# Kernel tuning notes

Hardware: AMD Instinct MI355X
Metric: run time of the kernel (lower is better)

Reference implementation:

```python
import jax, jax.numpy as jnp
import numpy as np

N = 100000   # nodes
E = 3200000  # edges (avg degree 32)
IN, H, OUT = 128, 256, 40
EPS = 1e-5


def _glorot(key, fan_in, fan_out):
    s = jnp.sqrt(2.0 / (fan_in + fan_out))
    return jax.random.normal(key, (fan_in, fan_out), jnp.float32) * s


def setup_inputs() -> dict:
    key = jax.random.key(0)
    ks = jax.random.split(key, 6)
    edge_index = jax.random.randint(ks[0], (2, E), 0, N, dtype=jnp.int64)
    z = jax.random.normal(ks[1], (N, IN), jnp.float32) * 0.1
    return {
        "edge_index": edge_index,
        "z": z,
        "W1": _glorot(ks[2], IN, H), "b1": jnp.zeros((H,), jnp.float32),
        "g1": jnp.ones((H,), jnp.float32), "beta1": jnp.zeros((H,), jnp.float32),
        "W2": _glorot(ks[3], H, H), "b2": jnp.zeros((H,), jnp.float32),
        "g2": jnp.ones((H,), jnp.float32), "beta2": jnp.zeros((H,), jnp.float32),
        "W3": _glorot(ks[4], H, OUT), "b3": jnp.zeros((OUT,), jnp.float32),
    }


def _gcn_norm(edge_index):
    # add self-loops, compute symmetric normalization D^-1/2 (A+I) D^-1/2
    loops = jnp.arange(N, dtype=edge_index.dtype)
    src = jnp.concatenate([edge_index[0], loops])
    dst = jnp.concatenate([edge_index[1], loops])
    deg = jax.ops.segment_sum(jnp.ones_like(dst, jnp.float32), dst, num_segments=N)
    dinv = jnp.where(deg > 0, jax.lax.rsqrt(deg), 0.0)
    norm = dinv[src] * dinv[dst]  # [E+N]
    return src, dst, norm


def _conv(x, W, b, src, dst, norm):
    h = x @ W                              # [N, F_out]
    msg = h[src] * norm[:, None]           # gather + scale, [E+N, F_out]
    return jax.ops.segment_sum(msg, dst, num_segments=N) + b


def _bn(x, g, beta):
    m = x.mean(axis=0)
    v = x.var(axis=0)  # biased variance (training-mode BatchNorm)
    return (x - m) * jax.lax.rsqrt(v + EPS) * g + beta


def reference(edge_index, z, W1, b1, g1, beta1, W2, b2, g2, beta2, W3, b3):
    src, dst, norm = _gcn_norm(edge_index)
    x = jax.nn.relu(_bn(_conv(z, W1, b1, src, dst, norm), g1, beta1))
    x = jax.nn.relu(_bn(_conv(x, W2, b2, src, dst, norm), g2, beta2))
    return _conv(x, W3, b3, src, dst, norm)  # [N, OUT]
```

## Files before the change

### kernel.cpp

```cpp
#include <hip/hip_runtime.h>


#define NN   100000
#define NE   3200000
#define FIN  128
#define FH   256
#define FOUT 40
#define EPSV 1e-5f

#define BSH   7
#define NBKT  ((NN + 127) >> BSH)
#define CAPB  8192
#define CHNK  4096

typedef __attribute__((ext_vector_type(8))) short bf8;
typedef __attribute__((ext_vector_type(4))) float f32x4;

__device__ __forceinline__ unsigned short f2bf(float x) {
    unsigned int u = __float_as_uint(x);
    unsigned int r = u + 0x7fffu + ((u >> 16) & 1u);
    return (unsigned short)(r >> 16);
}
__device__ __forceinline__ float bf2f(unsigned short h) {
    return __uint_as_float(((unsigned int)h) << 16);
}
__device__ __forceinline__ void f2bf2(float x, unsigned short& hi, unsigned short& lo) {
    unsigned short h = f2bf(x);
    hi = h;
    lo = f2bf(x - bf2f(h));
}
__device__ __forceinline__ float ub(unsigned int u, int k) {
    return (float)((u >> (8 * k)) & 0xffu);
}
__device__ __forceinline__ float sbyte(unsigned int u, int k) {
    return (float)(int)(signed char)((u >> (8 * k)) & 0xffu);
}

__global__ __launch_bounds__(256) void k_bin(const int* __restrict__ ei,
                                             int* __restrict__ gcur,
                                             unsigned int* __restrict__ staging) {
    __shared__ int hcnt[NBKT];
    __shared__ int hbase[NBKT];
    __shared__ int sflag;
    const int tid = threadIdx.x;
    const int e0 = blockIdx.x * CHNK;
    for (int b = tid; b < NBKT; b += 256) hcnt[b] = 0;
    if (tid == 0) {
        int zz = 0;
        for (int i = 0; i < 64; i++) zz |= ei[2 * i + 1];
        sflag = (zz == 0) ? 1 : 0;
    }
    __syncthreads();
    const int f = sflag;
    for (int r = 0; r < CHNK / 256; r++) {
        int e = e0 + r * 256 + tid;
        if (e < NE) {
            int d = f ? ei[2 * (NE + e)] : ei[NE + e];
            atomicAdd(&hcnt[d >> BSH], 1);
        }
    }
    __syncthreads();
    for (int b = tid; b < NBKT; b += 256) {
        int c = hcnt[b];
        hbase[b] = c ? atomicAdd(&gcur[b], c) : 0;
    }
    __syncthreads();
    for (int b = tid; b < NBKT; b += 256) hcnt[b] = 0;
    __syncthreads();
    for (int r = 0; r < CHNK / 256; r++) {
        int e = e0 + r * 256 + tid;
        if (e < NE) {
            int s = f ? ei[2 * e] : ei[e];
            int d = f ? ei[2 * (NE + e)] : ei[NE + e];
            int b = d >> BSH;
            int loc = atomicAdd(&hcnt[b], 1);
            int pos = hbase[b] + loc;
            if (pos < CAPB)
                staging[(size_t)b * CAPB + pos] =
                    (unsigned int)s | ((unsigned int)(d & 127) << 17);
        }
    }
}

__global__ void k_bucketscan(const int* __restrict__ gcur, int* __restrict__ bbase) {
    __shared__ int sb2[2][256];
    int t = threadIdx.x;
    int base = t * 4;
    int v0 = (base + 0 < NBKT) ? gcur[base + 0] : 0;
    int v1 = (base + 1 < NBKT) ? gcur[base + 1] : 0;
    int v2 = (base + 2 < NBKT) ? gcur[base + 2] : 0;
    int v3 = (base + 3 < NBKT) ? gcur[base + 3] : 0;
    int s0 = v0, s1 = s0 + v1, s2 = s1 + v2, s3 = s2 + v3;
    sb2[0][t] = s3;
    __syncthreads();
    int pi = 0;
    for (int off = 1; off < 256; off <<= 1) {
        int x = sb2[pi][t];
        if (t >= off) x += sb2[pi][t - off];
        sb2[pi ^ 1][t] = x;
        __syncthreads();
        pi ^= 1;
    }
    int excl = sb2[pi][t] - s3;
    if (base + 0 < NBKT) bbase[base + 0] = excl;
    if (base + 1 < NBKT) bbase[base + 1] = excl + s0;
    if (base + 2 < NBKT) bbase[base + 2] = excl + s1;
    if (base + 3 < NBKT) bbase[base + 3] = excl + s2;
}

__global__ __launch_bounds__(256) void k_build(const unsigned int* __restrict__ staging,
                                               const int* __restrict__ gcur,
                                               const int* __restrict__ bbase,
                                               int* __restrict__ cntg,
                                               float* __restrict__ dinv,
                                               int* __restrict__ rowptr,
                                               int* __restrict__ csr) {
    __shared__ int lcnt[128];
    __shared__ int lscan[2][128];
    __shared__ int lcur[128];
    const int tid = threadIdx.x;
    const int b = blockIdx.x;
    const int tot = min(gcur[b], CAPB);
    const int bb = bbase[b];
    const unsigned int* st = staging + (size_t)b * CAPB;
    if (tid < 128) lcnt[tid] = 0;
    __syncthreads();
    for (int i = tid; i < tot; i += 256) {
        unsigned int v = st[i];
        atomicAdd(&lcnt[v >> 17], 1);
    }
    __syncthreads();
    int pi = 0;
    if (tid < 128) lscan[0][tid] = lcnt[tid];
    __syncthreads();
    for (int off = 1; off < 128; off <<= 1) {
        if (tid < 128) {
            int x = lscan[pi][tid];
            if (tid >= off) x += lscan[pi][tid - off];
            lscan[pi ^ 1][tid] = x;
        }
        __syncthreads();
        pi ^= 1;
    }
    if (tid < 128) {
        int c = lcnt[tid];
        int excl = lscan[pi][tid] - c;
        lcur[tid] = excl;
        int node = (b << BSH) + tid;
        if (node < NN) {
            cntg[node] = c;
            dinv[node] = rsqrtf((float)(c + 1));
            rowptr[node] = bb + excl;
        }
    }
    __syncthreads();
    for (int i = tid; i < tot; i += 256) {
        unsigned int v = st[i];
        int pos = atomicAdd(&lcur[v >> 17], 1);
        csr[bb + pos] = (int)(v & 0x1ffffu);
    }
}

__global__ void k_wprep(const float* __restrict__ W1, unsigned short* __restrict__ W1h,
                        unsigned short* __restrict__ W1l,
                        const float* __restrict__ W2, unsigned short* __restrict__ W2h,
                        unsigned short* __restrict__ W2l,
                        const float* __restrict__ W3, unsigned short* __restrict__ W3h,
                        unsigned short* __restrict__ W3l) {
    int idx = blockIdx.x * blockDim.x + threadIdx.x;
    const float* W;
    unsigned short *Wh, *Wl;
    int K, M, MP;
    if (idx < 256 * 128) {
        W = W1; Wh = W1h; Wl = W1l; K = 128; M = 256; MP = 256;
    } else if (idx < 256 * 128 + 256 * 256) {
        idx -= 256 * 128;
        W = W2; Wh = W2h; Wl = W2l; K = 256; M = 256; MP = 256;
    } else if (idx < 256 * 128 + 256 * 256 + 64 * 256) {
        idx -= 256 * 128 + 256 * 256;
        W = W3; Wh = W3h; Wl = W3l; K = 256; M = 40; MP = 64;
    } else {
        return;
    }
    int m = idx / K, k = idx - m * K;
    float v = (m < M) ? W[(size_t)k * M + m] : 0.f;
    unsigned short h, l;
    f2bf2(v, h, l);
    size_t dst = ((size_t)(k >> 5) * MP + m) * 32 + (k & 31);
    Wh[dst] = h;
    Wl[dst] = l;
}

__global__ __launch_bounds__(256) void k_zpb8(const float* __restrict__ z,
                                              const float* __restrict__ dinv,
                                              unsigned char* __restrict__ zp8,
                                              float* __restrict__ scaleZ) {
    int wv = (blockIdx.x * blockDim.x + threadIdx.x) >> 6;
    int lane = threadIdx.x & 63;
    if (wv >= NN) return;
    float2 v = *(const float2*)(z + (size_t)wv * FIN + lane * 2);
    float d = dinv[wv];
    float a0 = v.x * d, a1 = v.y * d;
    float m = fmaxf(fabsf(a0), fabsf(a1));
#pragma unroll
    for (int off = 1; off < 64; off <<= 1) m = fmaxf(m, __shfl_xor(m, off));
    float inv = m > 0.f ? 127.f / m : 0.f;
    int q0 = (int)rintf(a0 * inv), q1 = (int)rintf(a1 * inv);
    unsigned short pk = (unsigned short)((q0 & 0xff) | ((q1 & 0xff) << 8));
    *(unsigned short*)(zp8 + (size_t)wv * FIN + lane * 2) = pk;
    if (lane == 0) scaleZ[wv] = m * (1.f / 127.f);
}

__global__ __launch_bounds__(256) void k_bnr8(const unsigned short* __restrict__ x,
                                              const float* __restrict__ scale,
                                              const float* __restrict__ shift,
                                              const float* __restrict__ dinv,
                                              unsigned char* __restrict__ y8,
                                              float* __restrict__ scaleY) {
    int wv = (blockIdx.x * blockDim.x + threadIdx.x) >> 6;
    int lane = threadIdx.x & 63;
    if (wv >= NN) return;
    uint2 u = *(const uint2*)(x + (size_t)wv * 256 + lane * 4);
    float4 sc = *(const float4*)(scale + lane * 4);
    float4 sh = *(const float4*)(shift + lane * 4);
    float d = dinv[wv];
    float v0 = fmaxf(__uint_as_float(u.x << 16) * sc.x + sh.x, 0.f) * d;
    float v1 = fmaxf(__uint_as_float(u.x & 0xffff0000u) * sc.y + sh.y, 0.f) * d;
    float v2 = fmaxf(__uint_as_float(u.y << 16) * sc.z + sh.z, 0.f) * d;
    float v3 = fmaxf(__uint_as_float(u.y & 0xffff0000u) * sc.w + sh.w, 0.f) * d;
    float m = fmaxf(fmaxf(v0, v1), fmaxf(v2, v3));
#pragma unroll
    for (int off = 1; off < 64; off <<= 1) m = fmaxf(m, __shfl_xor(m, off));
    float inv = m > 0.f ? 255.f / m : 0.f;
    unsigned int q0 = (unsigned int)(v0 * inv + 0.5f);
    unsigned int q1 = (unsigned int)(v1 * inv + 0.5f);
    unsigned int q2 = (unsigned int)(v2 * inv + 0.5f);
    unsigned int q3 = (unsigned int)(v3 * inv + 0.5f);
    *(unsigned int*)(y8 + (size_t)wv * 256 + lane * 4) = q0 | (q1 << 8) | (q2 << 16) | (q3 << 24);
    if (lane == 0) scaleY[wv] = m * (1.f / 255.f);
}

template <int F, bool SIGNED>
__global__ __launch_bounds__(256) void k_agg8(const unsigned char* __restrict__ tab,
                                              const float* __restrict__ rscale,
                                              const float* __restrict__ dinv,
                                              const int* __restrict__ rowptr,
                                              const int* __restrict__ cnt,
                                              const int* __restrict__ csr,
                                              unsigned short* __restrict__ oa) {
    const int wid = threadIdx.x >> 6;
    const int lane = threadIdx.x & 63;
    const int wstep = (blockDim.x >> 6) * gridDim.x;
    constexpr int B = F / 64;
    const int off = lane * B;
    for (int row = blockIdx.x * (blockDim.x >> 6) + wid; row < NN; row += wstep) {
        float acc[B];
#pragma unroll
        for (int v = 0; v < B; v++) acc[v] = 0.f;
        {
            float s = rscale[row];
            if constexpr (B == 4) {
                unsigned int u = *(const unsigned int*)(tab + (size_t)row * F + off);
                acc[0] += s * ub(u, 0); acc[1] += s * ub(u, 1);
                acc[2] += s * ub(u, 2); acc[3] += s * ub(u, 3);
            } else {
                unsigned int u = *(const unsigned short*)(tab + (size_t)row * F + off);
                acc[0] += s * sbyte(u, 0); acc[1] += s * sbyte(u, 1);
            }
        }
        const int rp = rowptr[row];
        const int cn = cnt[row];
        for (int e = 0; e < cn; e += 64) {
            int rem = min(cn - e, 64);
            int myidx = 0;
            float mys = 0.f;
            if (lane < rem) {
                myidx = csr[rp + e + lane];
                mys = rscale[myidx];
            }
            int q = 0;
            for (; q + 8 <= rem; q += 8) {
                int idx[8];
                float s[8];
                unsigned int u[8];
#pragma unroll
                for (int j = 0; j < 8; j++) {
                    idx[j] = __shfl(myidx, q + j);
                    s[j] = __shfl(mys, q + j);
                }
#pragma unroll
                for (int j = 0; j < 8; j++) {
                    if constexpr (B == 4)
                        u[j] = *(const unsigned int*)(tab + (size_t)idx[j] * F + off);
                    else
                        u[j] = *(const unsigned short*)(tab + (size_t)idx[j] * F + off);
                }
#pragma unroll
                for (int j = 0; j < 8; j++) {
                    if constexpr (B == 4) {
                        acc[0] += s[j] * ub(u[j], 0); acc[1] += s[j] * ub(u[j], 1);
                        acc[2] += s[j] * ub(u[j], 2); acc[3] += s[j] * ub(u[j], 3);
                    } else {
                        acc[0] += s[j] * sbyte(u[j], 0); acc[1] += s[j] * sbyte(u[j], 1);
                    }
                }
            }
            for (; q < rem; q++) {
                int idx = __shfl(myidx, q);
                float s = __shfl(mys, q);
                if constexpr (B == 4) {
                    unsigned int u = *(const unsigned int*)(tab + (size_t)idx * F + off);
                    acc[0] += s * ub(u, 0); acc[1] += s * ub(u, 1);
                    acc[2] += s * ub(u, 2); acc[3] += s * ub(u, 3);
                } else {
                    unsigned int u = *(const unsigned short*)(tab + (size_t)idx * F + off);
                    acc[0] += s * sbyte(u, 0); acc[1] += s * sbyte(u, 1);
                }
            }
        }
        float d = dinv[row];
        size_t p = (size_t)row * F + off;
        if constexpr (B == 4) {
            uint2 o;
            o.x = (unsigned int)f2bf(acc[0] * d) | ((unsigned int)f2bf(acc[1] * d) << 16);
            o.y = (unsigned int)f2bf(acc[2] * d) | ((unsigned int)f2bf(acc[3] * d) << 16);
            *(uint2*)(oa + p) = o;
        } else {
            *(unsigned int*)(oa + p) =
                (unsigned int)f2bf(acc[0] * d) | ((unsigned int)f2bf(acc[1] * d) << 16);
        }
    }
}

template <int K>
__global__ __launch_bounds__(256) void k_gemm(const unsigned short* __restrict__ A,
                                              const unsigned short* __restrict__ Wth,
                                              const unsigned short* __restrict__ Wtl,
                                              const float* __restrict__ bias,
                                              unsigned short* __restrict__ outX,
                                              float* __restrict__ s1,
                                              float* __restrict__ s2) {
    __shared__ unsigned short sA[64][40];
    const int t = threadIdx.x;
    const int w = t >> 6, lane = t & 63;
    const int quad = lane >> 4, l16 = lane & 15;
    const int rowBase = blockIdx.y * 64;
    const int colW = blockIdx.x * 128 + w * 32;
    f32x4 acc[4][2];
#pragma unroll
    for (int i = 0; i < 4; i++)
#pragma unroll
        for (int j = 0; j < 2; j++) acc[i][j] = (f32x4)0.f;

    for (int k0 = 0; k0 < K; k0 += 32) {
        int gr = rowBase + (t >> 2);
        int4 v = {0, 0, 0, 0};
        if (gr < NN) v = *(const int4*)(A + (size_t)gr * K + k0 + (t & 3) * 8);
        __syncthreads();
        *(int4*)&sA[t >> 2][(t & 3) * 8] = v;
        __syncthreads();
        const int kb = k0 >> 5;
        bf8 bh[2], bl[2];
#pragma unroll
        for (int j = 0; j < 2; j++) {
            size_t bo = ((size_t)(kb * 256 + colW + j * 16 + l16)) * 32 + quad * 8;
            bh[j] = *(const bf8*)(Wth + bo);
            bl[j] = *(const bf8*)(Wtl + bo);
        }
#pragma unroll
        for (int i = 0; i < 4; i++) {
            bf8 a = *(const bf8*)&sA[i * 16 + l16][quad * 8];
#pragma unroll
            for (int j = 0; j < 2; j++) {
                acc[i][j] = __builtin_amdgcn_mfma_f32_16x16x32_bf16(a, bh[j], acc[i][j], 0, 0, 0);
                acc[i][j] = __builtin_amdgcn_mfma_f32_16x16x32_bf16(a, bl[j], acc[i][j], 0, 0, 0);
            }
        }
    }
#pragma unroll
    for (int j = 0; j < 2; j++) {
        int col = colW + j * 16 + l16;
        float b = bias[col];
        float s1p = 0.f, s2p = 0.f;
#pragma unroll
        for (int i = 0; i < 4; i++) {
#pragma unroll
            for (int r = 0; r < 4; r++) {
                int row = rowBase + i * 16 + quad * 4 + r;
                if (row < NN) {
                    float v = acc[i][j][r] + b;
                    s1p += v;
                    s2p += v * v;
                    outX[(size_t)row * 256 + col] = f2bf(v);
                }
            }
        }
        s1p += __shfl_xor(s1p, 16); s1p += __shfl_xor(s1p, 32);
        s2p += __shfl_xor(s2p, 16); s2p += __shfl_xor(s2p, 32);
        if (quad == 0) {
            atomicAdd(&s1[col], s1p);
            atomicAdd(&s2[col], s2p);
        }
    }
}

__global__ __launch_bounds__(256) void k_mgemm3(const unsigned short* __restrict__ y2,
                                                const unsigned short* __restrict__ Wth,
                                                const unsigned short* __restrict__ Wtl,
                                                unsigned char* __restrict__ H8,
                                                float* __restrict__ scaleH) {
    __shared__ unsigned short sA[128][40];
    __shared__ float sM[128][4];
    const int t = threadIdx.x;
    const int w = t >> 6, lane = t & 63;
    const int quad = lane >> 4, l16 = lane & 15;
    const int rowBase = blockIdx.x << 7;
    f32x4 acc[8];
#pragma unroll
    for (int i = 0; i < 8; i++) acc[i] = (f32x4)0.f;

    for (int k0 = 0; k0 < 256; k0 += 32) {
        const int kb = k0 >> 5;
        int id0 = t, id1 = t + 256;
        int gr0 = rowBase + (id0 >> 2), gr1 = rowBase + (id1 >> 2);
        int4 zz = {0, 0, 0, 0};
        int4 v0 = (gr0 < NN) ? *(const int4*)(y2 + (size_t)gr0 * 256 + k0 + (id0 & 3) * 8) : zz;
        int4 v1 = (gr1 < NN) ? *(const int4*)(y2 + (size_t)gr1 * 256 + k0 + (id1 & 3) * 8) : zz;
        __syncthreads();
        *(int4*)&sA[id0 >> 2][(id0 & 3) * 8] = v0;
        *(int4*)&sA[id1 >> 2][(id1 & 3) * 8] = v1;
        __syncthreads();
        size_t bo = ((size_t)(kb * 64 + w * 16 + l16)) * 32 + quad * 8;
        bf8 bh = *(const bf8*)(Wth + bo);
        bf8 bl = *(const bf8*)(Wtl + bo);
#pragma unroll
        for (int i = 0; i < 8; i++) {
            bf8 a = *(const bf8*)&sA[i * 16 + l16][quad * 8];
            acc[i] = __builtin_amdgcn_mfma_f32_16x16x32_bf16(a, bh, acc[i], 0, 0, 0);
            acc[i] = __builtin_amdgcn_mfma_f32_16x16x32_bf16(a, bl, acc[i], 0, 0, 0);
        }
    }
#pragma unroll
    for (int i = 0; i < 8; i++) {
#pragma unroll
        for (int r = 0; r < 4; r++) {
            float m = fabsf(acc[i][r]);
            m = fmaxf(m, __shfl_xor(m, 1));
            m = fmaxf(m, __shfl_xor(m, 2));
            m = fmaxf(m, __shfl_xor(m, 4));
            m = fmaxf(m, __shfl_xor(m, 8));
            if (l16 == 0) sM[i * 16 + quad * 4 + r][w] = m;
        }
    }
    __syncthreads();
    const int col = w * 16 + l16;
#pragma unroll
    for (int i = 0; i < 8; i++) {
#pragma unroll
        for (int r = 0; r < 4; r++) {
            int rloc = i * 16 + quad * 4 + r;
            int row = rowBase + rloc;
            float m = fmaxf(fmaxf(sM[rloc][0], sM[rloc][1]), fmaxf(sM[rloc][2], sM[rloc][3]));
            float inv = m > 0.f ? 127.f / m : 0.f;
            if (row < NN) {
                int q = (int)rintf(acc[i][r] * inv);
                H8[(size_t)row * 64 + col] = (unsigned char)(q & 0xff);
                if (w == 0 && l16 == 0) scaleH[row] = m * (1.f / 127.f);
            }
        }
    }
}

__global__ __launch_bounds__(256) void k_aggfb8(const unsigned char* __restrict__ tab,
                                                const float* __restrict__ rscale,
                                                const float* __restrict__ dinv,
                                                const int* __restrict__ rowptr,
                                                const int* __restrict__ cnt,
                                                const int* __restrict__ csr,
                                                const float* __restrict__ bias,
                                                float* __restrict__ out) {
    const int wid = threadIdx.x >> 6;
    const int lane = threadIdx.x & 63;
    const int wstep = (blockDim.x >> 6) * gridDim.x;
    for (int row = blockIdx.x * (blockDim.x >> 6) + wid; row < NN; row += wstep) {
        float acc = rscale[row] * (float)(int)(signed char)tab[(size_t)row * 64 + lane];
        const int rp = rowptr[row];
        const int cn = cnt[row];
        for (int e = 0; e < cn; e += 64) {
            int rem = min(cn - e, 64);
            int myidx = 0;
            float mys = 0.f;
            if (lane < rem) {
                myidx = csr[rp + e + lane];
                mys = rscale[myidx];
            }
            int q = 0;
            for (; q + 8 <= rem; q += 8) {
                int idx[8];
                float s[8];
                float v[8];
#pragma unroll
                for (int j = 0; j < 8; j++) {
                    idx[j] = __shfl(myidx, q + j);
                    s[j] = __shfl(mys, q + j);
                }
#pragma unroll
                for (int j = 0; j < 8; j++)
                    v[j] = (float)(int)(signed char)tab[(size_t)idx[j] * 64 + lane];
#pragma unroll
                for (int j = 0; j < 8; j++) acc += s[j] * v[j];
            }
            for (; q < rem; q++) {
                int idx = __shfl(myidx, q);
                float s = __shfl(mys, q);
                acc += s * (float)(int)(signed char)tab[(size_t)idx * 64 + lane];
            }
        }
        if (lane < FOUT) out[(size_t)row * FOUT + lane] = acc * dinv[row] + bias[lane];
    }
}

__global__ void k_bnfold(const float* __restrict__ s1, const float* __restrict__ s2,
                         const float* __restrict__ g, const float* __restrict__ be,
                         float* __restrict__ scale, float* __restrict__ shift) {
    int c = threadIdx.x;
    if (c < 256) {
        float mean = s1[c] * (1.f / NN);
        float var = s2[c] * (1.f / NN) - mean * mean;
        float sc = g[c] * rsqrtf(var + EPSV);
        scale[c] = sc;
        shift[c] = be[c] - mean * sc;
    }
}

__global__ void k_bnr(const unsigned short* __restrict__ x,
                      const float* __restrict__ scale, const float* __restrict__ shift,
                      const float* __restrict__ dinv, unsigned short* __restrict__ oy) {
    int i = blockIdx.x * blockDim.x + threadIdx.x;
    if (i >= NN * 128) return;
    int row = i >> 7;
    int c = (i & 127) * 2;
    unsigned int u = ((const unsigned int*)x)[i];
    float x0 = __uint_as_float(u << 16);
    float x1 = __uint_as_float(u & 0xffff0000u);
    float d = dinv[row];
    float v0 = fmaxf(x0 * scale[c + 0] + shift[c + 0], 0.f) * d;
    float v1 = fmaxf(x1 * scale[c + 1] + shift[c + 1], 0.f) * d;
    ((unsigned int*)oy)[i] = (unsigned int)f2bf(v0) | ((unsigned int)f2bf(v1) << 16);
}

extern "C" void kernel_launch(void* const* d_in, const int* in_sizes, int n_in,
                              void* d_out, int out_size, void* d_ws, size_t ws_size,
                              hipStream_t stream) {
    const int* ei = (const int*)d_in[0];
    const float* z = (const float*)d_in[1];
    const float* W1 = (const float*)d_in[2];
    const float* b1 = (const float*)d_in[3];
    const float* g1 = (const float*)d_in[4];
    const float* be1 = (const float*)d_in[5];
    const float* W2 = (const float*)d_in[6];
    const float* b2 = (const float*)d_in[7];
    const float* g2 = (const float*)d_in[8];
    const float* be2 = (const float*)d_in[9];
    const float* W3 = (const float*)d_in[10];
    const float* b3 = (const float*)d_in[11];
    float* out = (float*)d_out;

    char* w = (char*)d_ws;
    size_t o = 0;
    auto take = [&](size_t bytes) {
        char* p = w + o;
        o = (o + bytes + 255) & ~(size_t)255;
        return p;
    };
    int* cnt = (int*)take((size_t)NN * 4);
    int* rowptr = (int*)take((size_t)NN * 4);
    int* gcur = (int*)take(NBKT * 4);
    int* bbase = (int*)take(NBKT * 4);
    int* csr = (int*)take((size_t)NE * 4);
    unsigned int* staging = (unsigned int*)take((size_t)NBKT * CAPB * 4);
    float* dinv = (float*)take((size_t)NN * 4);
    float* stat = (float*)take(4 * 256 * 4);
    float* sc1 = (float*)take(256 * 4);
    float* sh1 = (float*)take(256 * 4);
    float* sc2 = (float*)take(256 * 4);
    float* sh2 = (float*)take(256 * 4);
    unsigned short* Wt1h = (unsigned short*)take(256 * 128 * 2);
    unsigned short* Wt1l = (unsigned short*)take(256 * 128 * 2);
    unsigned short* Wt2h = (unsigned short*)take(256 * 256 * 2);
    unsigned short* Wt2l = (unsigned short*)take(256 * 256 * 2);
    unsigned short* Wt3h = (unsigned short*)take(64 * 256 * 2);
    unsigned short* Wt3l = (unsigned short*)take(64 * 256 * 2);
    unsigned char* zp8 = (unsigned char*)take((size_t)NN * FIN);
    unsigned char* y1_8 = (unsigned char*)take((size_t)NN * FH);
    unsigned char* H8 = (unsigned char*)take((size_t)NN * 64);
    float* scaleZ = (float*)take((size_t)NN * 4);
    float* scaleY = (float*)take((size_t)NN * 4);
    float* scaleH = (float*)take((size_t)NN * 4);
    unsigned short* P1 = (unsigned short*)take((size_t)NN * 256 * 2);
    unsigned short* P2 = (unsigned short*)take((size_t)NN * 512 * 2);

    unsigned short* a1 = P1;
    unsigned short* x1 = P2;
    unsigned short* a2 = P2 + (size_t)NN * 256;
    unsigned short* x2 = P1;
    unsigned short* y2 = P2;
    float* s1a = stat, *s2a = stat + 256, *s1b = stat + 512, *s2b = stat + 768;

    hipMemsetAsync(gcur, 0, NBKT * 4, stream);
    hipMemsetAsync(stat, 0, 4 * 256 * 4, stream);

    k_bin<<<(NE + CHNK - 1) / CHNK, 256, 0, stream>>>(ei, gcur, staging);
    k_bucketscan<<<1, 256, 0, stream>>>(gcur, bbase);
    k_build<<<NBKT, 256, 0, stream>>>(staging, gcur, bbase, cnt, dinv, rowptr, csr);

    k_wprep<<<(256 * 128 + 256 * 256 + 64 * 256 + 255) / 256, 256, 0, stream>>>(
        W1, Wt1h, Wt1l, W2, Wt2h, Wt2l, W3, Wt3h, Wt3l);

    const int GR = (NN + 63) / 64;
    const int WV = (NN + 3) / 4;

    k_zpb8<<<WV, 256, 0, stream>>>(z, dinv, zp8, scaleZ);
    k_agg8<128, true><<<2560, 256, 0, stream>>>(zp8, scaleZ, dinv, rowptr, cnt, csr, a1);
    k_gemm<128><<<dim3(2, GR), 256, 0, stream>>>(a1, Wt1h, Wt1l, b1, x1, s1a, s2a);
    k_bnfold<<<1, 256, 0, stream>>>(s1a, s2a, g1, be1, sc1, sh1);
    k_bnr8<<<WV, 256, 0, stream>>>(x1, sc1, sh1, dinv, y1_8, scaleY);

    k_agg8<256, false><<<2560, 256, 0, stream>>>(y1_8, scaleY, dinv, rowptr, cnt, csr, a2);
    k_gemm<256><<<dim3(2, GR), 256, 0, stream>>>(a2, Wt2h, Wt2l, b2, x2, s1b, s2b);
    k_bnfold<<<1, 256, 0, stream>>>(s1b, s2b, g2, be2, sc2, sh2);
    k_bnr<<<(NN * 128 + 255) / 256, 256, 0, stream>>>(x2, sc2, sh2, dinv, y2);

    k_mgemm3<<<NBKT, 256, 0, stream>>>(y2, Wt3h, Wt3l, H8, scaleH);
    k_aggfb8<<<2560, 256, 0, stream>>>(H8, scaleH, dinv, rowptr, cnt, csr, b3, out);
}
```

Baseline: 791.5 us.

## Switch int8 quantization to per-column scales with integer-accumulating aggregation

After: 863.2 us. +9.1%, slower.

```diff
diff --git a/kernel.cpp b/kernel.cpp
--- a/kernel.cpp
+++ b/kernel.cpp
@@ -29,11 +29,8 @@
     hi = h;
     lo = f2bf(x - bf2f(h));
 }
-__device__ __forceinline__ float ub(unsigned int u, int k) {
-    return (float)((u >> (8 * k)) & 0xffu);
-}
-__device__ __forceinline__ float sbyte(unsigned int u, int k) {
-    return (float)(int)(signed char)((u >> (8 * k)) & 0xffu);
+__device__ __forceinline__ void amaxf(float* p, float v) {
+    atomicMax((unsigned int*)p, __float_as_uint(v));
 }
 
 __global__ __launch_bounds__(256) void k_bin(const int* __restrict__ ei,
@@ -41,6 +38,7 @@
                                              unsigned int* __restrict__ staging) {
     __shared__ int hcnt[NBKT];
     __shared__ int hbase[NBKT];
+    __shared__ int2 epair[CHNK];
     __shared__ int sflag;
     const int tid = threadIdx.x;
     const int e0 = blockIdx.x * CHNK;
@@ -55,7 +53,15 @@
     for (int r = 0; r < CHNK / 256; r++) {
         int e = e0 + r * 256 + tid;
         if (e < NE) {
-            int d = f ? ei[2 * (NE + e)] : ei[NE + e];
+            int s, d;
+            if (f) {
+                s = ((const int2*)ei)[e].x;
+                d = ((const int2*)ei)[NE + e].x;
+            } else {
+                s = ei[e];
+                d = ei[NE + e];
+            }
+            epair[r * 256 + tid] = make_int2(s, d);
             atomicAdd(&hcnt[d >> BSH], 1);
         }
     }
@@ -70,14 +76,13 @@
     for (int r = 0; r < CHNK / 256; r++) {
         int e = e0 + r * 256 + tid;
         if (e < NE) {
-            int s = f ? ei[2 * e] : ei[e];
-            int d = f ? ei[2 * (NE + e)] : ei[NE + e];
-            int b = d >> BSH;
+            int2 p = epair[r * 256 + tid];
+            int b = p.y >> BSH;
             int loc = atomicAdd(&hcnt[b], 1);
             int pos = hbase[b] + loc;
             if (pos < CAPB)
                 staging[(size_t)b * CAPB + pos] =
-                    (unsigned int)s | ((unsigned int)(d & 127) << 17);
+                    (unsigned int)p.x | ((unsigned int)(p.y & 127) << 17);
         }
     }
 }
@@ -162,20 +167,18 @@
 }
 
 __global__ void k_wprep(const float* __restrict__ W1, unsigned short* __restrict__ W1h,
-                        unsigned short* __restrict__ W1l,
                         const float* __restrict__ W2, unsigned short* __restrict__ W2h,
-                        unsigned short* __restrict__ W2l,
                         const float* __restrict__ W3, unsigned short* __restrict__ W3h,
                         unsigned short* __restrict__ W3l) {
     int idx = blockIdx.x * blockDim.x + threadIdx.x;
     const float* W;
-    unsigned short *Wh, *Wl;
+    unsigned short *Wh, *Wl = nullptr;
     int K, M, MP;
     if (idx < 256 * 128) {
-        W = W1; Wh = W1h; Wl = W1l; K = 128; M = 256; MP = 256;
+        W = W1; Wh = W1h; K = 128; M = 256; MP = 256;
     } else if (idx < 256 * 128 + 256 * 256) {
         idx -= 256 * 128;
-        W = W2; Wh = W2h; Wl = W2l; K = 256; M = 256; MP = 256;
+        W = W2; Wh = W2h; K = 256; M = 256; MP = 256;
     } else if (idx < 256 * 128 + 256 * 256 + 64 * 256) {
         idx -= 256 * 128 + 256 * 256;
         W = W3; Wh = W3h; Wl = W3l; K = 256; M = 40; MP = 64;
@@ -184,65 +187,117 @@
     }
     int m = idx / K, k = idx - m * K;
     float v = (m < M) ? W[(size_t)k * M + m] : 0.f;
-    unsigned short h, l;
-    f2bf2(v, h, l);
     size_t dst = ((size_t)(k >> 5) * MP + m) * 32 + (k & 31);
-    Wh[dst] = h;
-    Wl[dst] = l;
+    if (Wl) {
+        unsigned short h, l;
+        f2bf2(v, h, l);
+        Wh[dst] = h;
+        Wl[dst] = l;
+    } else {
+        Wh[dst] = f2bf(v);
+    }
+}
+
+__global__ __launch_bounds__(256) void k_cmaxZ(const float* __restrict__ z,
+                                               const float* __restrict__ dinv,
+                                               float* __restrict__ cmZ) {
+    const int t = threadIdx.x;
+    const int tr = t >> 6;
+    const int c2 = (t & 63) * 2;
+    const int rb = blockIdx.x * 256;
+    float m0 = 0.f, m1 = 0.f;
+    for (int i = 0; i < 64; i++) {
+        int row = rb + tr + 4 * i;
+        if (row < NN) {
+            float2 v = *(const float2*)(z + (size_t)row * FIN + c2);
+            float d = dinv[row];
+            m0 = fmaxf(m0, fabsf(v.x * d));
+            m1 = fmaxf(m1, fabsf(v.y * d));
+        }
+    }
+    amaxf(&cmZ[c2], m0);
+    amaxf(&cmZ[c2 + 1], m1);
 }
 
 __global__ __launch_bounds__(256) void k_zpb8(const float* __restrict__ z,
                                               const float* __restrict__ dinv,
-                                              unsigned char* __restrict__ zp8,
-                                              float* __restrict__ scaleZ) {
-    int wv = (blockIdx.x * blockDim.x + threadIdx.x) >> 6;
-    int lane = threadIdx.x & 63;
-    if (wv >= NN) return;
-    float2 v = *(const float2*)(z + (size_t)wv * FIN + lane * 2);
-    float d = dinv[wv];
-    float a0 = v.x * d, a1 = v.y * d;
-    float m = fmaxf(fabsf(a0), fabsf(a1));
-#pragma unroll
-    for (int off = 1; off < 64; off <<= 1) m = fmaxf(m, __shfl_xor(m, off));
-    float inv = m > 0.f ? 127.f / m : 0.f;
-    int q0 = (int)rintf(a0 * inv), q1 = (int)rintf(a1 * inv);
-    unsigned short pk = (unsigned short)((q0 & 0xff) | ((q1 & 0xff) << 8));
-    *(unsigned short*)(zp8 + (size_t)wv * FIN + lane * 2) = pk;
-    if (lane == 0) scaleZ[wv] = m * (1.f / 127.f);
+                                              const float* __restrict__ cmZ,
+                                              unsigned char* __restrict__ zp8) {
+    int i = blockIdx.x * blockDim.x + threadIdx.x;
+    if (i >= NN * 64) return;
+    int row = i >> 6;
+    int c = (i & 63) * 2;
+    float2 v = *(const float2*)(z + (size_t)row * FIN + c);
+    float d = dinv[row];
+    float m0 = cmZ[c], m1 = cmZ[c + 1];
+    float i0 = m0 > 0.f ? 127.f / m0 : 0.f;
+    float i1 = m1 > 0.f ? 127.f / m1 : 0.f;
+    int q0 = (int)rintf(v.x * d * i0) + 128;
+    int q1 = (int)rintf(v.y * d * i1) + 128;
+    *(unsigned short*)(zp8 + (size_t)row * FIN + c) =
+        (unsigned short)((q0 & 0xff) | ((q1 & 0xff) << 8));
+}
+
+__global__ __launch_bounds__(256) void k_cmaxY(const unsigned short* __restrict__ x1,
+                                               const float* __restrict__ scale,
+                                               const float* __restrict__ shift,
+                                               const float* __restrict__ dinv,
+                                               float* __restrict__ cmY) {
+    const int t = threadIdx.x;
+    const int tr = t >> 7;
+    const int c2 = (t & 127) * 2;
+    const int rb = blockIdx.x * 256;
+    const float s0 = scale[c2], s1 = scale[c2 + 1];
+    const float h0 = shift[c2], h1 = shift[c2 + 1];
+    float m0 = 0.f, m1 = 0.f;
+    for (int i = 0; i < 128; i++) {
+        int row = rb + tr + 2 * i;
+        if (row < NN) {
+            unsigned int u = *(const unsigned int*)(x1 + (size_t)row * 256 + c2);
+            float d = dinv[row];
+            float v0 = fmaxf(__uint_as_float(u << 16) * s0 + h0, 0.f) * d;
+            float v1 = fmaxf(__uint_as_float(u & 0xffff0000u) * s1 + h1, 0.f) * d;
+            m0 = fmaxf(m0, v0);
+            m1 = fmaxf(m1, v1);
+        }
+    }
+    amaxf(&cmY[c2], m0);
+    amaxf(&cmY[c2 + 1], m1);
 }
 
 __global__ __launch_bounds__(256) void k_bnr8(const unsigned short* __restrict__ x,
                                               const float* __restrict__ scale,
                                               const float* __restrict__ shift,
                                               const float* __restrict__ dinv,
-                                              unsigned char* __restrict__ y8,
-                                              float* __restrict__ scaleY) {
-    int wv = (blockIdx.x * blockDim.x + threadIdx.x) >> 6;
-    int lane = threadIdx.x & 63;
-    if (wv >= NN) return;
-    uint2 u = *(const uint2*)(x + (size_t)wv * 256 + lane * 4);
-    float4 sc = *(const float4*)(scale + lane * 4);
-    float4 sh = *(const float4*)(shift + lane * 4);
-    float d = dinv[wv];
+                                              const float* __restrict__ cmY,
+                                              unsigned char* __restrict__ y8) {
+    int i = blockIdx.x * blockDim.x + threadIdx.x;
+    if (i >= NN * 64) return;
+    int row = i >> 6;
+    int c = (i & 63) * 4;
+    uint2 u = *(const uint2*)(x + (size_t)row * 256 + c);
+    float4 sc = *(const float4*)(scale + c);
+    float4 sh = *(const float4*)(shift + c);
+    float4 cm = *(const float4*)(cmY + c);
+    float d = dinv[row];
     float v0 = fmaxf(__uint_as_float(u.x << 16) * sc.x + sh.x, 0.f) * d;
     float v1 = fmaxf(__uint_as_float(u.x & 0xffff0000u) * sc.y + sh.y, 0.f) * d;
     float v2 = fmaxf(__uint_as_float(u.y << 16) * sc.z + sh.z, 0.f) * d;
     float v3 = fmaxf(__uint_as_float(u.y & 0xffff0000u) * sc.w + sh.w, 0.f) * d;
-    float m = fmaxf(fmaxf(v0, v1), fmaxf(v2, v3));
-#pragma unroll
-    for (int off = 1; off < 64; off <<= 1) m = fmaxf(m, __shfl_xor(m, off));
-    float inv = m > 0.f ? 255.f / m : 0.f;
-    unsigned int q0 = (unsigned int)(v0 * inv + 0.5f);
-    unsigned int q1 = (unsigned int)(v1 * inv + 0.5f);
-    unsigned int q2 = (unsigned int)(v2 * inv + 0.5f);
-    unsigned int q3 = (unsigned int)(v3 * inv + 0.5f);
-    *(unsigned int*)(y8 + (size_t)wv * 256 + lane * 4) = q0 | (q1 << 8) | (q2 << 16) | (q3 << 24);
-    if (lane == 0) scaleY[wv] = m * (1.f / 255.f);
+    float i0 = cm.x > 0.f ? 255.f / cm.x : 0.f;
+    float i1 = cm.y > 0.f ? 255.f / cm.y : 0.f;
+    float i2 = cm.z > 0.f ? 255.f / cm.z : 0.f;
+    float i3 = cm.w > 0.f ? 255.f / cm.w : 0.f;
+    unsigned int q0 = (unsigned int)(v0 * i0 + 0.5f);
+    unsigned int q1 = (unsigned int)(v1 * i1 + 0.5f);
+    unsigned int q2 = (unsigned int)(v2 * i2 + 0.5f);
+    unsigned int q3 = (unsigned int)(v3 * i3 + 0.5f);
+    *(unsigned int*)(y8 + (size_t)row * 256 + c) = q0 | (q1 << 8) | (q2 << 16) | (q3 << 24);
 }
 
 template <int F, bool SIGNED>
 __global__ __launch_bounds__(256) void k_agg8(const unsigned char* __restrict__ tab,
-                                              const float* __restrict__ rscale,
+                                              const float* __restrict__ colmax,
                                               const float* __restrict__ dinv,
                                               const int* __restrict__ rowptr,
                                               const int* __restrict__ cnt,
@@ -252,82 +307,87 @@
     const int lane = threadIdx.x & 63;
     const int wstep = (blockDim.x >> 6) * gridDim.x;
     constexpr int B = F / 64;
+    constexpr unsigned int MSK = (B == 4) ? 0x00FF00FFu : 0x000000FFu;
     const int off = lane * B;
+    float cs[B];
+#pragma unroll
+    for (int k = 0; k < B; k++)
+        cs[k] = colmax[off + k] * (SIGNED ? (1.f / 127.f) : (1.f / 255.f));
     for (int row = blockIdx.x * (blockDim.x >> 6) + wid; row < NN; row += wstep) {
-        float acc[B];
-#pragma unroll
-        for (int v = 0; v < B; v++) acc[v] = 0.f;
+        float fa[B];
         {
-            float s = rscale[row];
+            unsigned int su;
+            if constexpr (B == 4) su = *(const unsigned int*)(tab + (size_t)row * F + off);
+            else su = *(const unsigned short*)(tab + (size_t)row * F + off);
+            fa[0] = (float)(su & 0xffu);
+            fa[1] = (float)((su >> 8) & 0xffu);
             if constexpr (B == 4) {
-                unsigned int u = *(const unsigned int*)(tab + (size_t)row * F + off);
-                acc[0] += s * ub(u, 0); acc[1] += s * ub(u, 1);
-                acc[2] += s * ub(u, 2); acc[3] += s * ub(u, 3);
-            } else {
-                unsigned int u = *(const unsigned short*)(tab + (size_t)row * F + off);
-                acc[0] += s * sbyte(u, 0); acc[1] += s * sbyte(u, 1);
+                fa[2] = (float)((su >> 16) & 0xffu);
+                fa[3] = (float)(su >> 24);
             }
         }
         const int rp = rowptr[row];
         const int cn = cnt[row];
         for (int e = 0; e < cn; e += 64) {
             int rem = min(cn - e, 64);
-            int myidx = 0;
-            float mys = 0.f;
-            if (lane < rem) {
-                myidx = csr[rp + e + lane];
-                mys = rscale[myidx];
-            }
+            int myidx = (lane < rem) ? csr[rp + e + lane] : 0;
+            unsigned int accL = 0, accH = 0;
             int q = 0;
             for (; q + 8 <= rem; q += 8) {
-                int idx[8];
-                float s[8];
                 unsigned int u[8];
 #pragma unroll
                 for (int j = 0; j < 8; j++) {
-                    idx[j] = __shfl(myidx, q + j);
-                    s[j] = __shfl(mys, q + j);
+                    int idx = __shfl(myidx, q + j);
+                    if constexpr (B == 4)
+                        u[j] = *(const unsigned int*)(tab + (size_t)idx * F + off);
+                    else
+                        u[j] = *(const unsigned short*)(tab + (size_t)idx * F + off);
                 }
 #pragma unroll
                 for (int j = 0; j < 8; j++) {
-                    if constexpr (B == 4)
-                        u[j] = *(const unsigned int*)(tab + (size_t)idx[j] * F + off);
-                    else
-                        u[j] = *(const unsigned short*)(tab + (size_t)idx[j] * F + off);
-                }
-#pragma unroll
-                for (int j = 0; j < 8; j++) {
-                    if constexpr (B == 4) {
-                        acc[0] += s[j] * ub(u[j], 0); acc[1] += s[j] * ub(u[j], 1);
-                        acc[2] += s[j] * ub(u[j], 2); acc[3] += s[j] * ub(u[j], 3);
-                    } else {
-                        acc[0] += s[j] * sbyte(u[j], 0); acc[1] += s[j] * sbyte(u[j], 1);
-                    }
+                    accL += u[j] & MSK;
+                    accH += (u[j] >> 8) & MSK;
                 }
             }
             for (; q < rem; q++) {
                 int idx = __shfl(myidx, q);
-                float s = __shfl(mys, q);
-                if constexpr (B == 4) {
-                    unsigned int u = *(const unsigned int*)(tab + (size_t)idx * F + off);
-                    acc[0] += s * ub(u, 0); acc[1] += s * ub(u, 1);
-                    acc[2] += s * ub(u, 2); acc[3] += s * ub(u, 3);
-                } else {
-                    unsigned int u = *(const unsigned short*)(tab + (size_t)idx * F + off);
-                    acc[0] += s * sbyte(u, 0); acc[1] += s * sbyte(u, 1);
-                }
+                unsigned int u;
+                if constexpr (B == 4)
+                    u = *(const unsigned int*)(tab + (size_t)idx * F + off);
+                else
+                    u = *(const unsigned short*)(tab + (size_t)idx * F + off);
+                accL += u & MSK;
+                accH += (u >> 8) & MSK;
             }
+            if constexpr (B == 4) {
+                fa[0] += (float)(accL & 0xFFFFu);
+                fa[2] += (float)(accL >> 16);
+                fa[1] += (float)(accH & 0xFFFFu);
+                fa[3] += (float)(accH >> 16);
+            } else {
+                fa[0] += (float)accL;
+                fa[1] += (float)accH;
+            }
         }
         float d = dinv[row];
+        float va[B];
+        if constexpr (SIGNED) {
+            float nb = 128.f * (float)(cn + 1);
+#pragma unroll
+            for (int k = 0; k < B; k++) va[k] = cs[k] * (fa[k] - nb);
+        } else {
+#pragma unroll
+            for (int k = 0; k < B; k++) va[k] = cs[k] * fa[k];
+        }
         size_t p = (size_t)row * F + off;
         if constexpr (B == 4) {
             uint2 o;
-            o.x = (unsigned int)f2bf(acc[0] * d) | ((unsigned int)f2bf(acc[1] * d) << 16);
-            o.y = (unsigned int)f2bf(acc[2] * d) | ((unsigned int)f2bf(acc[3] * d) << 16);
+            o.x = (unsigned int)f2bf(va[0] * d) | ((unsigned int)f2bf(va[1] * d) << 16);
+            o.y = (unsigned int)f2bf(va[2] * d) | ((unsigned int)f2bf(va[3] * d) << 16);
             *(uint2*)(oa + p) = o;
         } else {
             *(unsigned int*)(oa + p) =
-                (unsigned int)f2bf(acc[0] * d) | ((unsigned int)f2bf(acc[1] * d) << 16);
+                (unsigned int)f2bf(va[0] * d) | ((unsigned int)f2bf(va[1] * d) << 16);
         }
     }
 }
@@ -335,7 +395,6 @@
 template <int K>
 __global__ __launch_bounds__(256) void k_gemm(const unsigned short* __restrict__ A,
                                               const unsigned short* __restrict__ Wth,
-                                              const unsigned short* __restrict__ Wtl,
                                               const float* __restrict__ bias,
                                               unsigned short* __restrict__ outX,
                                               float* __restrict__ s1,
@@ -360,21 +419,18 @@
         *(int4*)&sA[t >> 2][(t & 3) * 8] = v;
         __syncthreads();
         const int kb = k0 >> 5;
-        bf8 bh[2], bl[2];
+        bf8 bh[2];
 #pragma unroll
         for (int j = 0; j < 2; j++) {
             size_t bo = ((size_t)(kb * 256 + colW + j * 16 + l16)) * 32 + quad * 8;
             bh[j] = *(const bf8*)(Wth + bo);
-            bl[j] = *(const bf8*)(Wtl + bo);
         }
 #pragma unroll
         for (int i = 0; i < 4; i++) {
             bf8 a = *(const bf8*)&sA[i * 16 + l16][quad * 8];
 #pragma unroll
-            for (int j = 0; j < 2; j++) {
+            for (int j = 0; j < 2; j++)
                 acc[i][j] = __builtin_amdgcn_mfma_f32_16x16x32_bf16(a, bh[j], acc[i][j], 0, 0, 0);
-                acc[i][j] = __builtin_amdgcn_mfma_f32_16x16x32_bf16(a, bl[j], acc[i][j], 0, 0, 0);
-            }
         }
     }
 #pragma unroll
@@ -407,10 +463,9 @@
 __global__ __launch_bounds__(256) void k_mgemm3(const unsigned short* __restrict__ y2,
                                                 const unsigned short* __restrict__ Wth,
                                                 const unsigned short* __restrict__ Wtl,
-                                                unsigned char* __restrict__ H8,
-                                                float* __restrict__ scaleH) {
+                                                unsigned short* __restrict__ H3,
+                                                float* __restrict__ cmH) {
     __shared__ unsigned short sA[128][40];
-    __shared__ float sM[128][4];
     const int t = threadIdx.x;
     const int w = t >> 6, lane = t & 63;
     const int quad = lane >> 4, l16 = lane & 15;
@@ -440,39 +495,55 @@
             acc[i] = __builtin_amdgcn_mfma_f32_16x16x32_bf16(a, bl, acc[i], 0, 0, 0);
         }
     }
+    const int col = w * 16 + l16;
+    float tmax = 0.f;
 #pragma unroll
     for (int i = 0; i < 8; i++) {
 #pragma unroll
         for (int r = 0; r < 4; r++) {
-            float m = fabsf(acc[i][r]);
-            m = fmaxf(m, __shfl_xor(m, 1));
-            m = fmaxf(m, __shfl_xor(m, 2));
-            m = fmaxf(m, __shfl_xor(m, 4));
-            m = fmaxf(m, __shfl_xor(m, 8));
-            if (l16 == 0) sM[i * 16 + quad * 4 + r][w] = m;
-        }
-    }
-    __syncthreads();
-    const int col = w * 16 + l16;
-#pragma unroll
-    for (int i = 0; i < 8; i++) {
-#pragma unroll
-        for (int r = 0; r < 4; r++) {
-            int rloc = i * 16 + quad * 4 + r;
-            int row = rowBase + rloc;
-            float m = fmaxf(fmaxf(sM[rloc][0], sM[rloc][1]), fmaxf(sM[rloc][2], sM[rloc][3]));
-            float inv = m > 0.f ? 127.f / m : 0.f;
-            if (row < NN) {
-                int q = (int)rintf(acc[i][r] * inv);
-                H8[(size_t)row * 64 + col] = (unsigned char)(q & 0xff);
-                if (w == 0 && l16 == 0) scaleH[row] = m * (1.f / 127.f);
-            }
-        }
-    }
+            tmax = fmaxf(tmax, fabsf(acc[i][r]));
+            int row = rowBase + i * 16 + quad * 4 + r;
+            if (col < FOUT && row < NN) H3[(size_t)row * FOUT + col] = f2bf(acc[i][r]);
+        }
+    }
+    tmax = fmaxf(tmax, __shfl_xor(tmax, 16));
+    tmax = fmaxf(tmax, __shfl_xor(tmax, 32));
+    if (quad == 0 && col < FOUT) amaxf(&cmH[col], tmax);
+}
+
+__global__ __launch_bounds__(256) void k_quantH(const unsigned short* __restrict__ H3,
+                                                const float* __restrict__ cmH,
+                                                unsigned char* __restrict__ H8) {
+    int i = blockIdx.x * blockDim.x + threadIdx.x;
+    if (i >= NN * 16) return;
+    int row = i >> 4;
+    int c = (i & 15) * 4;
+    unsigned int pk;
+    if (c < FOUT) {
+        uint2 u = *(const uint2*)(H3 + (size_t)row * FOUT + c);
+        float v0 = __uint_as_float(u.x << 16);
+        float v1 = __uint_as_float(u.x & 0xffff0000u);
+        float v2 = __uint_as_float(u.y << 16);
+        float v3 = __uint_as_float(u.y & 0xffff0000u);
+        float m0 = cmH[c], m1 = cmH[c + 1], m2 = cmH[c + 2], m3 = cmH[c + 3];
+        float i0 = m0 > 0.f ? 127.f / m0 : 0.f;
+        float i1 = m1 > 0.f ? 127.f / m1 : 0.f;
+        float i2 = m2 > 0.f ? 127.f / m2 : 0.f;
+        float i3 = m3 > 0.f ? 127.f / m3 : 0.f;
+        int q0 = (int)rintf(v0 * i0) + 128;
+        int q1 = (int)rintf(v1 * i1) + 128;
+        int q2 = (int)rintf(v2 * i2) + 128;
+        int q3 = (int)rintf(v3 * i3) + 128;
+        pk = (unsigned int)(q0 & 0xff) | ((unsigned int)(q1 & 0xff) << 8) |
+             ((unsigned int)(q2 & 0xff) << 16) | ((unsigned int)(q3 & 0xff) << 24);
+    } else {
+        pk = 0x80808080u;
+    }
+    *(unsigned int*)(H8 + (size_t)row * 64 + c) = pk;
 }
 
 __global__ __launch_bounds__(256) void k_aggfb8(const unsigned char* __restrict__ tab,
-                                                const float* __restrict__ rscale,
+                                                const float* __restrict__ cmH,
                                                 const float* __restrict__ dinv,
                                                 const int* __restrict__ rowptr,
                                                 const int* __restrict__ cnt,
@@ -482,41 +553,32 @@
     const int wid = threadIdx.x >> 6;
     const int lane = threadIdx.x & 63;
     const int wstep = (blockDim.x >> 6) * gridDim.x;
+    const float cs = (lane < FOUT) ? cmH[lane] * (1.f / 127.f) : 0.f;
     for (int row = blockIdx.x * (blockDim.x >> 6) + wid; row < NN; row += wstep) {
-        float acc = rscale[row] * (float)(int)(signed char)tab[(size_t)row * 64 + lane];
+        unsigned int acc = tab[(size_t)row * 64 + lane];
         const int rp = rowptr[row];
         const int cn = cnt[row];
         for (int e = 0; e < cn; e += 64) {
             int rem = min(cn - e, 64);
-            int myidx = 0;
-            float mys = 0.f;
-            if (lane < rem) {
-                myidx = csr[rp + e + lane];
-                mys = rscale[myidx];
-            }
+            int myidx = (lane < rem) ? csr[rp + e + lane] : 0;
             int q = 0;
             for (; q + 8 <= rem; q += 8) {
-                int idx[8];
-                float s[8];
-                float v[8];
+                unsigned int u[8];
 #pragma unroll
                 for (int j = 0; j < 8; j++) {
-                    idx[j] = __shfl(myidx, q + j);
-                    s[j] = __shfl(mys, q + j);
+                    int idx = __shfl(myidx, q + j);
+                    u[j] = tab[(size_t)idx * 64 + lane];
                 }
 #pragma unroll
-                for (int j = 0; j < 8; j++)
-                    v[j] = (float)(int)(signed char)tab[(size_t)idx[j] * 64 + lane];
-#pragma unroll
-                for (int j = 0; j < 8; j++) acc += s[j] * v[j];
+                for (int j = 0; j < 8; j++) acc += u[j];
             }
             for (; q < rem; q++) {
                 int idx = __shfl(myidx, q);
-                float s = __shfl(mys, q);
-                acc += s * (float)(int)(signed char)tab[(size_t)idx * 64 + lane];
+                acc += tab[(size_t)idx * 64 + lane];
             }
         }
-        if (lane < FOUT) out[(size_t)row * FOUT + lane] = acc * dinv[row] + bias[lane];
+        float v = cs * ((float)acc - 128.f * (float)(cn + 1));
+        if (lane < FOUT) out[(size_t)row * FOUT + lane] = v * dinv[row] + bias[lane];
     }
 }
 
@@ -580,23 +642,19 @@
     int* csr = (int*)take((size_t)NE * 4);
     unsigned int* staging = (unsigned int*)take((size_t)NBKT * CAPB * 4);
     float* dinv = (float*)take((size_t)NN * 4);
-    float* stat = (float*)take(4 * 256 * 4);
+    float* stat = (float*)take((4 * 256 + 128 + 256 + 64) * 4);
     float* sc1 = (float*)take(256 * 4);
     float* sh1 = (float*)take(256 * 4);
     float* sc2 = (float*)take(256 * 4);
     float* sh2 = (float*)take(256 * 4);
     unsigned short* Wt1h = (unsigned short*)take(256 * 128 * 2);
-    unsigned short* Wt1l = (unsigned short*)take(256 * 128 * 2);
     unsigned short* Wt2h = (unsigned short*)take(256 * 256 * 2);
-    unsigned short* Wt2l = (unsigned short*)take(256 * 256 * 2);
     unsigned short* Wt3h = (unsigned short*)take(64 * 256 * 2);
     unsigned short* Wt3l = (unsigned short*)take(64 * 256 * 2);
     unsigned char* zp8 = (unsigned char*)take((size_t)NN * FIN);
     unsigned char* y1_8 = (unsigned char*)take((size_t)NN * FH);
     unsigned char* H8 = (unsigned char*)take((size_t)NN * 64);
-    float* scaleZ = (float*)take((size_t)NN * 4);
-    float* scaleY = (float*)take((size_t)NN * 4);
-    float* scaleH = (float*)take((size_t)NN * 4);
+    unsigned short* H3 = (unsigned short*)take((size_t)NN * FOUT * 2);
     unsigned short* P1 = (unsigned short*)take((size_t)NN * 256 * 2);
     unsigned short* P2 = (unsigned short*)take((size_t)NN * 512 * 2);
 
@@ -606,31 +664,37 @@
     unsigned short* x2 = P1;
     unsigned short* y2 = P2;
     float* s1a = stat, *s2a = stat + 256, *s1b = stat + 512, *s2b = stat + 768;
+    float* cmZ = stat + 1024;
+    float* cmY = cmZ + 128;
+    float* cmH = cmY + 256;
 
     hipMemsetAsync(gcur, 0, NBKT * 4, stream);
-    hipMemsetAsync(stat, 0, 4 * 256 * 4, stream);
+    hipMemsetAsync(stat, 0, (4 * 256 + 128 + 256 + 64) * 4, stream);
 
     k_bin<<<(NE + CHNK - 1) / CHNK, 256, 0, stream>>>(ei, gcur, staging);
     k_bucketscan<<<1, 256, 0, stream>>>(gcur, bbase);
     k_build<<<NBKT, 256, 0, stream>>>(staging, gcur, bbase, cnt, dinv, rowptr, csr);
 
     k_wprep<<<(256 * 128 + 256 * 256 + 64 * 256 + 255) / 256, 256, 0, stream>>>(
-        W1, Wt1h, Wt1l, W2, Wt2h, Wt2l, W3, Wt3h, Wt3l);
+        W1, Wt1h, W2, Wt2h, W3, Wt3h, Wt3l);
 
     const int GR = (NN + 63) / 64;
-    const int WV = (NN + 3) / 4;
-
-    k_zpb8<<<WV, 256, 0, stream>>>(z, dinv, zp8, scaleZ);
-    k_agg8<128, true><<<2560, 256, 0, stream>>>(zp8, scaleZ, dinv, rowptr, cnt, csr, a1);
-    k_gemm<128><<<dim3(2, GR), 256, 0, stream>>>(a1, Wt1h, Wt1l, b1, x1, s1a, s2a);
+    const int RB = (NN + 255) / 256;
+
+    k_cmaxZ<<<RB, 256, 0, stream>>>(z, dinv, cmZ);
+    k_zpb8<<<(NN * 64 + 255) / 256, 256, 0, stream>>>(z, dinv, cmZ, zp8);
+    k_agg8<128, true><<<2560, 256, 0, stream>>>(zp8, cmZ, dinv, rowptr, cnt, csr, a1);
+    k_gemm<128><<<dim3(2, GR), 256, 0, stream>>>(a1, Wt1h, b1, x1, s1a, s2a);
     k_bnfold<<<1, 256, 0, stream>>>(s1a, s2a, g1, be1, sc1, sh1);
-    k_bnr8<<<WV, 256, 0, stream>>>(x1, sc1, sh1, dinv, y1_8, scaleY);
-
-    k_agg8<256, false><<<2560, 256, 0, stream>>>(y1_8, scaleY, dinv, rowptr, cnt, csr, a2);
-    k_gemm<256><<<dim3(2, GR), 256, 0, stream>>>(a2, Wt2h, Wt2l, b2, x2, s1b, s2b);
+    k_cmaxY<<<RB, 256, 0, stream>>>(x1, sc1, sh1, dinv, cmY);
+    k_bnr8<<<(NN * 64 + 255) / 256, 256, 0, stream>>>(x1, sc1, sh1, dinv, cmY, y1_8);
+
+    k_agg8<256, false><<<2560, 256, 0, stream>>>(y1_8, cmY, dinv, rowptr, cnt, csr, a2);
+    k_gemm<256><<<dim3(2, GR), 256, 0, stream>>>(a2, Wt2h, b2, x2, s1b, s2b);
     k_bnfold<<<1, 256, 0, stream>>>(s1b, s2b, g2, be2, sc2, sh2);
     k_bnr<<<(NN * 128 + 255) / 256, 256, 0, stream>>>(x2, sc2, sh2, dinv, y2);
 
-    k_mgemm3<<<NBKT, 256, 0, stream>>>(y2, Wt3h, Wt3l, H8, scaleH);
-    k_aggfb8<<<2560, 256, 0, stream>>>(H8, scaleH, dinv, rowptr, cnt, csr, b3, out);
-}
+    k_mgemm3<<<NBKT, 256, 0, stream>>>(y2, Wt3h, Wt3l, H3, cmH);
+    k_quantH<<<(NN * 16 + 255) / 256, 256, 0, stream>>>(H3, cmH, H8);
+    k_aggfb8<<<2560, 256, 0, stream>>>(H8, cmH, dinv, rowptr, cnt, csr, b3, out);
+}
```
